# Optimization experiments

Measured on AMD Instinct MI355X. Metric: run time of the kernel, lower is better.

The kernel has to match this reference:

```python
import jax, jax.numpy as jnp
import numpy as np

N_NODES = 200000
N_EDGES = 800000
N_GRAPHS = 4096
IN_FEAT = 64
CONV_SIZES = [128, 128, 256, 256]
MAX_DEGREE = 5  # buckets 0..5 (degree clamped)
N_CLASSES = 2


def setup_inputs() -> dict:
    key = jax.random.key(0)
    ks = jax.random.split(key, 32)
    inp = {}
    inp["x"] = jax.random.normal(ks[0], (N_NODES, IN_FEAT), dtype=jnp.float32)
    inp["edge_index"] = jax.random.randint(ks[1], (2, N_EDGES), 0, N_NODES, dtype=jnp.int32)
    inp["batch"] = jnp.sort(jax.random.randint(ks[2], (N_NODES,), 0, N_GRAPHS, dtype=jnp.int32))
    # per-layer MFConv params: Wl (neighbor-sum branch, with bias), Wr (root branch, no bias),
    # one linear per degree bucket -> leading dim MAX_DEGREE+1
    c_in = IN_FEAT
    k = 3
    for li, c_out in enumerate(CONV_SIZES):
        s = 1.0 / np.sqrt(c_in)
        inp[f"Wl{li}"] = jax.random.normal(ks[k], (MAX_DEGREE + 1, c_in, c_out), dtype=jnp.float32) * s; k += 1
        inp[f"bl{li}"] = jax.random.normal(ks[k], (MAX_DEGREE + 1, c_out), dtype=jnp.float32) * 0.01; k += 1
        inp[f"Wr{li}"] = jax.random.normal(ks[k], (MAX_DEGREE + 1, c_in, c_out), dtype=jnp.float32) * s; k += 1
        c_in = c_out
    in_final = sum(CONV_SIZES) + CONV_SIZES[-1]  # concat of all layer outputs + pooled last layer
    inp["Wf"] = jax.random.normal(ks[k], (in_final, N_CLASSES), dtype=jnp.float32) * (1.0 / np.sqrt(in_final)); k += 1
    inp["bf"] = jax.random.normal(ks[k], (N_CLASSES,), dtype=jnp.float32) * 0.01
    return inp


def _mfconv(x, src, dst, deg, Wl, bl, Wr):
    # neighbor sum aggregation (source_to_target flow): msg_i = sum_{j->i} x_j
    msg = jax.ops.segment_sum(x[src], dst, num_segments=x.shape[0])  # [N, c_in]
    out = jnp.zeros((x.shape[0], Wl.shape[2]), dtype=x.dtype)
    for d in range(Wl.shape[0]):  # small fixed loop over degree buckets
        r = msg @ Wl[d] + bl[d] + x @ Wr[d]
        out = jnp.where((deg == d)[:, None], r, out)
    return out


def reference(x, edge_index, batch,
              Wl0, bl0, Wr0, Wl1, bl1, Wr1, Wl2, bl2, Wr2, Wl3, bl3, Wr3,
              Wf, bf):
    src, dst = edge_index[0], edge_index[1]
    n = x.shape[0]
    deg = jnp.clip(jnp.zeros((n,), jnp.int32).at[dst].add(1), 0, MAX_DEGREE)
    hs = []
    h = x
    for Wl, bl, Wr in ((Wl0, bl0, Wr0), (Wl1, bl1, Wr1), (Wl2, bl2, Wr2), (Wl3, bl3, Wr3)):
        h = _mfconv(h, src, dst, deg, Wl, bl, Wr)
        hs.append(h)
    # global_add_pool then repeat_interleave back to nodes == gather pooled by batch id
    h_pool = jax.ops.segment_sum(h, batch, num_segments=N_GRAPHS)  # [G, c_last]
    h_pool_ = h_pool[batch]  # [N, c_last]
    h_cat = jnp.concatenate(hs + [h_pool_], axis=1)  # [N, sum(sizes)+c_last]
    logits = h_cat @ Wf + bf
    return jax.nn.softmax(logits, axis=1)
```

## Files before the change

### kernel.cpp

```cpp
#include <hip/hip_runtime.h>
#include <cstdint>
#include <cstddef>

namespace {

constexpr int NN   = 200000;
constexpr int NE   = 800000;
constexpr int NG   = 4096;
constexpr int MAXD = 5;

constexpr int BM = 64;
constexpr int NBC = (NN + 255) / 256;
constexpr int NBLK  = (NN + BM - 1) / BM + 6;
constexpr int PERMN = NBLK * BM;

typedef _Float16 half8 __attribute__((ext_vector_type(8)));
typedef _Float16 half4 __attribute__((ext_vector_type(4)));
typedef _Float16 half2 __attribute__((ext_vector_type(2)));
typedef float    f32x4 __attribute__((ext_vector_type(4)));

constexpr size_t P_L0 = (size_t)6 * 128 * 128;
constexpr size_t P_L1 = (size_t)6 * 256 * 128;
constexpr size_t P_L2 = (size_t)6 * 256 * 256;
constexpr size_t P_L3 = (size_t)6 * 512 * 256;
constexpr size_t O_P0 = 0;
constexpr size_t O_P1 = O_P0 + P_L0;
constexpr size_t O_P2 = O_P1 + P_L1;
constexpr size_t O_P3 = O_P2 + P_L2;
constexpr size_t WTOT = O_P3 + P_L3;


__global__ void k_memset32(int* __restrict__ p, int v, int n) {
    int i = blockIdx.x * 256 + threadIdx.x;
    if (i < n) p[i] = v;
}

__global__ void k_report(float* __restrict__ outp, float v, int n) {
    int i = blockIdx.x * 256 + threadIdx.x;
    if (i < n) outp[i] = v;
}

template <int CIN, int COUT>
__global__ void k_wpack(const float* __restrict__ Wl, const float* __restrict__ Wr,
                        _Float16* __restrict__ hi, _Float16* __restrict__ lo) {
    constexpr int NT = CIN / 16;
    constexpr int NB = COUT / 16;
    const int total = 6 * NT * NB * 64;
    int idx = blockIdx.x * 256 + threadIdx.x;
    if (idx >= total) return;
    const int lane = idx & 63;
    int rest = idx >> 6;
    const int nb = rest % NB; rest /= NB;
    const int ti = rest % NT;
    const int d  = rest / NT;
    const int k0 = ti * 32 + ((lane >> 4) * 8);
    const int n  = nb * 16 + (lane & 15);
    half8 hv, lv;
#pragma unroll
    for (int j = 0; j < 8; j++) {
        const int kk = k0 + j;
        const float v = (kk < CIN)
                            ? Wl[((size_t)d * CIN + kk) * COUT + n]
                            : Wr[((size_t)d * CIN + (kk - CIN)) * COUT + n];
        const _Float16 h = (_Float16)v;
        hv[j] = h;
        lv[j] = (_Float16)(v - (float)h);
    }
    *(half8*)(hi + (size_t)idx * 8) = hv;
    *(half8*)(lo + (size_t)idx * 8) = lv;
}


__global__ void k_count_deg(const int* __restrict__ dst, int* __restrict__ deg) {
    int e = blockIdx.x * 256 + threadIdx.x;
    if (e < NE) atomicAdd(&deg[dst[e]], 1);
}

__global__ void k_scan_part(const int* __restrict__ deg, int* __restrict__ part) {
    __shared__ int s[256];
    int t = threadIdx.x, i = blockIdx.x * 256 + t;
    s[t] = (i < NN) ? deg[i] : 0;
    __syncthreads();
    for (int st = 128; st > 0; st >>= 1) {
        if (t < st) s[t] += s[t + st];
        __syncthreads();
    }
    if (t == 0) part[blockIdx.x] = s[0];
}

__global__ void k_scan_single(int* __restrict__ part, int nb) {
    __shared__ int s[1024];
    int t = threadIdx.x;
    int v0 = (t < nb) ? part[t] : 0;
    s[t] = v0;
    __syncthreads();
    for (int off = 1; off < 1024; off <<= 1) {
        int v = (t >= off) ? s[t - off] : 0;
        __syncthreads();
        s[t] += v;
        __syncthreads();
    }
    if (t < nb) part[t] = s[t] - v0;
}

__global__ void k_scan_final(const int* __restrict__ deg, const int* __restrict__ part,
                             int* __restrict__ row_ptr, int* __restrict__ cursor) {
    __shared__ int s[256];
    int t = threadIdx.x, i = blockIdx.x * 256 + t;
    int v0 = (i < NN) ? deg[i] : 0;
    s[t] = v0;
    __syncthreads();
    for (int off = 1; off < 256; off <<= 1) {
        int v = (t >= off) ? s[t - off] : 0;
        __syncthreads();
        s[t] += v;
        __syncthreads();
    }
    if (i < NN) {
        int excl = s[t] - v0 + part[blockIdx.x];
        row_ptr[i] = excl;
        cursor[i]  = excl;
        if (i == NN - 1) row_ptr[NN] = excl + v0;
    }
}

__global__ void k_fill_csr(const int* __restrict__ src, const int* __restrict__ dst,
                           int* __restrict__ cursor, int* __restrict__ col) {
    int e = blockIdx.x * 256 + threadIdx.x;
    if (e < NE) {
        int d = dst[e];
        int slot = atomicAdd(&cursor[d], 1);
        col[slot] = src[e];
    }
}


__global__ void k_bucket_blockcount(const int* __restrict__ deg, int* __restrict__ blkcnt) {
    __shared__ int h[6];
    int t = threadIdx.x;
    if (t < 6) h[t] = 0;
    __syncthreads();
    int i = blockIdx.x * 256 + t;
    if (i < NN) atomicAdd(&h[min(deg[i], MAXD)], 1);
    __syncthreads();
    if (t < 6) blkcnt[t * NBC + blockIdx.x] = h[t];
}

__global__ void k_bucket_scanall(int* __restrict__ blkcnt, int* __restrict__ bpad) {
    __shared__ int tot[6];
    int t = threadIdx.x;
    if (t < 6) {
        int run = 0;
        for (int j = 0; j < NBC; j++) {
            int v = blkcnt[t * NBC + j];
            blkcnt[t * NBC + j] = run;
            run += v;
        }
        tot[t] = run;
    }
    __syncthreads();
    if (t == 0) {
        int off = 0;
        for (int b = 0; b < 6; b++) {
            bpad[b] = off;
            off += ((tot[b] + BM - 1) / BM) * BM;
        }
        bpad[6] = off;
    }
}

__global__ void k_scatter2(const int* __restrict__ deg, const int* __restrict__ blkcnt,
                           const int* __restrict__ bpad, int* __restrict__ perm) {
    __shared__ int base[6];
    int t = threadIdx.x;
    if (t < 6) base[t] = bpad[t] + blkcnt[t * NBC + blockIdx.x];
    __syncthreads();
    int i = blockIdx.x * 256 + t;
    if (i < NN) {
        int b = min(deg[i], MAXD);
        int pos = atomicAdd(&base[b], 1);
        perm[pos] = i;
    }
}


__global__ void k_aggregate128(const float* __restrict__ hin, const int* __restrict__ row_ptr,
                               const int* __restrict__ col, float* __restrict__ msg) {
    int node = blockIdx.x * 4 + (threadIdx.x >> 6);
    int lane = threadIdx.x & 63;
    int s = row_ptr[node], e = row_ptr[node + 1];
    float2 acc = make_float2(0.f, 0.f);
    int p = s;
    for (; p + 4 <= e; p += 4) {
        const int c0 = col[p], c1 = col[p + 1], c2 = col[p + 2], c3 = col[p + 3];
        const float2 v0 = *(const float2*)(hin + (size_t)c0 * 128 + lane * 2);
        const float2 v1 = *(const float2*)(hin + (size_t)c1 * 128 + lane * 2);
        const float2 v2 = *(const float2*)(hin + (size_t)c2 * 128 + lane * 2);
        const float2 v3 = *(const float2*)(hin + (size_t)c3 * 128 + lane * 2);
        acc.x += (v0.x + v1.x) + (v2.x + v3.x);
        acc.y += (v0.y + v1.y) + (v2.y + v3.y);
    }
    for (; p < e; p++) {
        const float2 v = *(const float2*)(hin + (size_t)col[p] * 128 + lane * 2);
        acc.x += v.x; acc.y += v.y;
    }
    *(float2*)(msg + (size_t)node * 128 + lane * 2) = acc;
}

template <int C0, int C1, int COUT, int MINW, bool POOL_FUSE>
__launch_bounds__(512, MINW)
__global__ void k_transform(const float* __restrict__ hin0, const float* __restrict__ hin1,
                            const int* __restrict__ row_ptr, const int* __restrict__ col,
                            const _Float16* __restrict__ wph, const _Float16* __restrict__ wpl,
                            const float* __restrict__ bias, const float* __restrict__ Wf,
                            const int* __restrict__ perm, const int* __restrict__ deg,
                            const int* __restrict__ batch,
                            float* __restrict__ out0, float* __restrict__ pool,
                            float* __restrict__ logits, int wf_off) {
    constexpr int CIN = C0 + C1;
    constexpr int NW  = CIN / 32;
    constexpr int NT  = 2 * NW;
    constexpr int NB  = COUT / 16;
    constexpr int NTN = NB / 8;
    constexpr int CPL = CIN / 64;
    constexpr int PB_R = POOL_FUSE ? 64 : 1;

    struct FragBuf {
        _Float16 Ah[NW][4][64][8];
        _Float16 Al[NW][4][64][8];
    };
    union SMemU {
        FragBuf f;
        float pbuf[PB_R][COUT];
    };
    __shared__ SMemU sm;
    __shared__ int rowid[BM];
    __shared__ int gb[BM];
    __shared__ float lsx[BM], lsy[BM];

    const int t  = threadIdx.x;
    const int m0 = blockIdx.x * BM;

    if (t < BM) {
        rowid[t] = perm[m0 + t];
        lsx[t] = 0.f; lsy[t] = 0.f;
    }
    __syncthreads();
    if (rowid[0] < 0) return;

    const int d = min(deg[rowid[0]], MAXD);

    const int am = t & 63, wv = t >> 6;

    if constexpr (POOL_FUSE) {
        if (t < BM) gb[t] = (rowid[t] >= 0) ? batch[rowid[t]] : -1;
    }

    {
        const int kk = CPL * am;
        const bool lo_half = (C1 == 0) || (kk < C0);
        const float* gsrc = lo_half ? hin0 : hin1;
        const int    gst  = lo_half ? C0 : C1;
        const int    goff = lo_half ? kk : (kk - C0);
        const int ti = kk >> 5;
        const int o  = (kk >> 3) & 3;
        const int j0 = kk & 7;

#pragma unroll
        for (int i = 0; i < 8; i++) {
            const int r = wv * 8 + i;
            const int node = rowid[r];
            float a0 = 0.f, a1 = 0.f, a2 = 0.f, a3 = 0.f;
            if (node >= 0) {
                const int es = row_ptr[node], ee = row_ptr[node + 1];
                int p = es;
                for (; p + 4 <= ee; p += 4) {
                    const int c0 = col[p], c1 = col[p + 1];
                    const int c2 = col[p + 2], c3 = col[p + 3];
                    const float* r0 = gsrc + (size_t)c0 * gst + goff;
                    const float* r1 = gsrc + (size_t)c1 * gst + goff;
                    const float* r2 = gsrc + (size_t)c2 * gst + goff;
                    const float* r3 = gsrc + (size_t)c3 * gst + goff;
                    if constexpr (CPL == 4) {
                        f32x4 v0 = *(const f32x4*)r0, v1 = *(const f32x4*)r1;
                        f32x4 v2 = *(const f32x4*)r2, v3 = *(const f32x4*)r3;
                        v0 += v1; v2 += v3; v0 += v2;
                        a0 += v0[0]; a1 += v0[1]; a2 += v0[2]; a3 += v0[3];
                    } else if constexpr (CPL == 2) {
                        float2 v0 = *(const float2*)r0, v1 = *(const float2*)r1;
                        float2 v2 = *(const float2*)r2, v3 = *(const float2*)r3;
                        a0 += (v0.x + v1.x) + (v2.x + v3.x);
                        a1 += (v0.y + v1.y) + (v2.y + v3.y);
                    } else {
                        a0 += (*r0 + *r1) + (*r2 + *r3);
                    }
                }
                for (; p < ee; p++) {
                    const float* rr = gsrc + (size_t)col[p] * gst + goff;
                    if constexpr (CPL == 4) {
                        f32x4 v = *(const f32x4*)rr;
                        a0 += v[0]; a1 += v[1]; a2 += v[2]; a3 += v[3];
                    } else if constexpr (CPL == 2) {
                        float2 v = *(const float2*)rr;
                        a0 += v.x; a1 += v.y;
                    } else {
                        a0 += *rr;
                    }
                }
            }
            const int mt = r >> 4, rl = r & 15;
            if constexpr (CPL == 4) {
                half4 hv, lv;
                hv[0] = (_Float16)a0; lv[0] = (_Float16)(a0 - (float)hv[0]);
                hv[1] = (_Float16)a1; lv[1] = (_Float16)(a1 - (float)hv[1]);
                hv[2] = (_Float16)a2; lv[2] = (_Float16)(a2 - (float)hv[2]);
                hv[3] = (_Float16)a3; lv[3] = (_Float16)(a3 - (float)hv[3]);
                *(half4*)&sm.f.Ah[ti][mt][rl + 16 * o][j0] = hv;
                *(half4*)&sm.f.Al[ti][mt][rl + 16 * o][j0] = lv;
            } else if constexpr (CPL == 2) {
                half2 hv, lv;
                hv[0] = (_Float16)a0; lv[0] = (_Float16)(a0 - (float)hv[0]);
                hv[1] = (_Float16)a1; lv[1] = (_Float16)(a1 - (float)hv[1]);
                *(half2*)&sm.f.Ah[ti][mt][rl + 16 * o][j0] = hv;
                *(half2*)&sm.f.Al[ti][mt][rl + 16 * o][j0] = lv;
            } else {
                const _Float16 h = (_Float16)a0;
                sm.f.Ah[ti][mt][rl + 16 * o][j0] = h;
                sm.f.Al[ti][mt][rl + 16 * o][j0] = (_Float16)(a0 - (float)h);
            }
        }
    }
    __syncthreads();

    const int lx = t & 15, qd = (t >> 4) & 3;
    const int nb0 = wv * NTN;
    int rnode[4];
#pragma unroll
    for (int mt = 0; mt < 4; mt++) rnode[mt] = rowid[(am & 15) + 16 * mt];

    f32x4 acc[4][NTN];
#pragma unroll
    for (int mt = 0; mt < 4; mt++)
#pragma unroll
        for (int nt = 0; nt < NTN; nt++) acc[mt][nt] = (f32x4)0.f;

    for (int ti = 0; ti < NW; ti++) {
        half8 bh[NTN], bl[NTN];
        const size_t tbase = (((size_t)d * NT + ti) * NB) * 512;
#pragma unroll
        for (int nt = 0; nt < NTN; nt++) {
            const size_t off = tbase + (size_t)(nb0 + nt) * 512 + (size_t)am * 8;
            bh[nt] = *(const half8*)(wph + off);
            bl[nt] = *(const half8*)(wpl + off);
        }
        half8 ah[4], alo[4];
#pragma unroll
        for (int mt = 0; mt < 4; mt++) {
            ah[mt]  = *(const half8*)&sm.f.Ah[ti][mt][am][0];
            alo[mt] = *(const half8*)&sm.f.Al[ti][mt][am][0];
        }
#pragma unroll
        for (int nt = 0; nt < NTN; nt++)
#pragma unroll
            for (int mt = 0; mt < 4; mt++) {
                acc[mt][nt] = __builtin_amdgcn_mfma_f32_16x16x32_f16(ah[mt],  bh[nt], acc[mt][nt], 0, 0, 0);
                acc[mt][nt] = __builtin_amdgcn_mfma_f32_16x16x32_f16(alo[mt], bh[nt], acc[mt][nt], 0, 0, 0);
                acc[mt][nt] = __builtin_amdgcn_mfma_f32_16x16x32_f16(ah[mt],  bl[nt], acc[mt][nt], 0, 0, 0);
            }
    }
    for (int ti = NW; ti < NT; ti++) {
        half8 bh[NTN], bl[NTN];
        const size_t tbase = (((size_t)d * NT + ti) * NB) * 512;
#pragma unroll
        for (int nt = 0; nt < NTN; nt++) {
            const size_t off = tbase + (size_t)(nb0 + nt) * 512 + (size_t)am * 8;
            bh[nt] = *(const half8*)(wph + off);
            bl[nt] = *(const half8*)(wpl + off);
        }
        const int e = (ti - NW) * 32 + 8 * (am >> 4);
        f32x4 ra[4], rb[4];
#pragma unroll
        for (int mt = 0; mt < 4; mt++) {
            ra[mt] = (f32x4)0.f; rb[mt] = (f32x4)0.f;
            if (rnode[mt] >= 0) {
                const float* r = (C1 == 0 || e < C0)
                                     ? hin0 + (size_t)rnode[mt] * C0 + e
                                     : hin1 + (size_t)rnode[mt] * C1 + (e - C0);
                ra[mt] = *(const f32x4*)r;
                rb[mt] = *(const f32x4*)(r + 4);
            }
        }
        half8 ah[4], alo[4];
#pragma unroll
        for (int mt = 0; mt < 4; mt++) {
#pragma unroll
            for (int i = 0; i < 4; i++) {
                const _Float16 h0 = (_Float16)ra[mt][i];
                ah[mt][i] = h0;
                alo[mt][i] = (_Float16)(ra[mt][i] - (float)h0);
                const _Float16 h1 = (_Float16)rb[mt][i];
                ah[mt][4 + i] = h1;
                alo[mt][4 + i] = (_Float16)(rb[mt][i] - (float)h1);
            }
        }
#pragma unroll
        for (int nt = 0; nt < NTN; nt++)
#pragma unroll
            for (int mt = 0; mt < 4; mt++) {
                acc[mt][nt] = __builtin_amdgcn_mfma_f32_16x16x32_f16(ah[mt],  bh[nt], acc[mt][nt], 0, 0, 0);
                acc[mt][nt] = __builtin_amdgcn_mfma_f32_16x16x32_f16(alo[mt], bh[nt], acc[mt][nt], 0, 0, 0);
                acc[mt][nt] = __builtin_amdgcn_mfma_f32_16x16x32_f16(ah[mt],  bl[nt], acc[mt][nt], 0, 0, 0);
            }
    }

    float blv[NTN], w0[NTN], w1[NTN];
    int cols[NTN];
#pragma unroll
    for (int nt = 0; nt < NTN; nt++) {
        cols[nt] = wv * (16 * NTN) + nt * 16 + lx;
        blv[nt] = bias[d * COUT + cols[nt]];
        w0[nt]  = Wf[(size_t)(wf_off + cols[nt]) * 2 + 0];
        w1[nt]  = Wf[(size_t)(wf_off + cols[nt]) * 2 + 1];
    }

    __syncthreads();

#pragma unroll
    for (int mt = 0; mt < 4; mt++)
#pragma unroll
    for (int r = 0; r < 4; r++) {
        const int ri = mt * 16 + qd * 4 + r;
        const int node = rowid[ri];
        float p0 = 0.f, p1 = 0.f;
        float h[NTN];
#pragma unroll
        for (int nt = 0; nt < NTN; nt++) h[nt] = 0.f;
        if (node >= 0) {
#pragma unroll
            for (int nt = 0; nt < NTN; nt++) {
                h[nt] = acc[mt][nt][r] + blv[nt];
                p0 = fmaf(h[nt], w0[nt], p0);
                p1 = fmaf(h[nt], w1[nt], p1);
            }
            if constexpr (!POOL_FUSE) {
                float* orow = out0 + (size_t)node * COUT;
#pragma unroll
                for (int nt = 0; nt < NTN; nt++) orow[cols[nt]] = h[nt];
            }
        }
        if constexpr (POOL_FUSE) {
#pragma unroll
            for (int nt = 0; nt < NTN; nt++) sm.pbuf[ri][cols[nt]] = h[nt];
        }
#pragma unroll
        for (int s = 1; s < 16; s <<= 1) {
            p0 += __shfl_xor(p0, s, 64);
            p1 += __shfl_xor(p1, s, 64);
        }
        if (node >= 0 && lx == 0) {
            atomicAdd(&lsx[ri], p0);
            atomicAdd(&lsy[ri], p1);
        }
    }
    __syncthreads();

    if (t < BM) {
        const int node = rowid[t];
        if (node >= 0) {
            logits[(size_t)node * 2 + 0] += lsx[t];
            logits[(size_t)node * 2 + 1] += lsy[t];
        }
    }

    if constexpr (POOL_FUSE) {
        const int c  = t & 255;
        const int rh = t >> 8;
        float run = 0.f;
        int rg = -1;
        const int r0 = rh * 32, r1 = r0 + 32;
        for (int r = r0; r < r1; r++) {
            const int g = gb[r];
            if (g != rg) {
                if (rg >= 0) atomicAdd(&pool[(size_t)rg * 256 + c], run);
                run = 0.f; rg = g;
            }
            if (g >= 0) run += sm.pbuf[r][c];
        }
        if (rg >= 0) atomicAdd(&pool[(size_t)rg * 256 + c], run);
    }
}


__launch_bounds__(512, 4)
__global__ void k_gemm2b(float* __restrict__ buf0, float* __restrict__ buf1,
                         const _Float16* __restrict__ wph, const _Float16* __restrict__ wpl,
                         const float* __restrict__ bias, const float* __restrict__ Wf,
                         const int* __restrict__ perm, const int* __restrict__ deg,
                         float* __restrict__ logits) {
    constexpr int COUT = 256, NT = 8, NB = 16, NTN = 2;
    __shared__ _Float16 Ah[NT][4][64][8];
    __shared__ _Float16 Al[NT][4][64][8];
    __shared__ int rowid[BM];
    __shared__ float lsx[BM], lsy[BM];

    const int t  = threadIdx.x;
    const int m0 = blockIdx.x * BM;

    if (t < BM) {
        rowid[t] = perm[m0 + t];
        lsx[t] = 0.f; lsy[t] = 0.f;
    }
    __syncthreads();
    if (rowid[0] < 0) return;

    const int d = min(deg[rowid[0]], MAXD);

    const int am = t & 63, wv = t >> 6;

    {
        const int kk = 4 * am;
        const float* gsrc = (am < 32) ? buf0 : buf1;
        const int    goff = (am < 32) ? kk : (kk - 128);
        const int ti = am >> 3;
        const int o  = (am >> 1) & 3;
        const int j0 = 4 * (am & 1);
#pragma unroll
        for (int i = 0; i < 8; i++) {
            const int r = wv * 8 + i;
            const int node = rowid[r];
            f32x4 v = (f32x4)0.f;
            if (node >= 0) v = *(const f32x4*)(gsrc + (size_t)node * 128 + goff);
            const int mt = r >> 4, rl = r & 15;
            half4 hv, lv;
#pragma unroll
            for (int c = 0; c < 4; c++) {
                const _Float16 h = (_Float16)v[c];
                hv[c] = h; lv[c] = (_Float16)(v[c] - (float)h);
            }
            *(half4*)&Ah[ti][mt][rl + 16 * o][j0] = hv;
            *(half4*)&Al[ti][mt][rl + 16 * o][j0] = lv;
        }
    }
    __syncthreads();

    const int lx = t & 15, qd = (t >> 4) & 3;
    const int nb0 = wv * NTN;

    f32x4 acc[4][NTN];
#pragma unroll
    for (int mt = 0; mt < 4; mt++)
#pragma unroll
        for (int nt = 0; nt < NTN; nt++) acc[mt][nt] = (f32x4)0.f;

    for (int ti = 0; ti < NT; ti++) {
        half8 bh[NTN], bl[NTN];
        const size_t tbase = (((size_t)d * NT + ti) * NB) * 512;
#pragma unroll
        for (int nt = 0; nt < NTN; nt++) {
            const size_t off = tbase + (size_t)(nb0 + nt) * 512 + (size_t)am * 8;
            bh[nt] = *(const half8*)(wph + off);
            bl[nt] = *(const half8*)(wpl + off);
        }
        half8 ah[4], alo[4];
#pragma unroll
        for (int mt = 0; mt < 4; mt++) {
            ah[mt]  = *(const half8*)&Ah[ti][mt][am][0];
            alo[mt] = *(const half8*)&Al[ti][mt][am][0];
        }
#pragma unroll
        for (int nt = 0; nt < NTN; nt++)
#pragma unroll
            for (int mt = 0; mt < 4; mt++) {
                acc[mt][nt] = __builtin_amdgcn_mfma_f32_16x16x32_f16(ah[mt],  bh[nt], acc[mt][nt], 0, 0, 0);
                acc[mt][nt] = __builtin_amdgcn_mfma_f32_16x16x32_f16(alo[mt], bh[nt], acc[mt][nt], 0, 0, 0);
                acc[mt][nt] = __builtin_amdgcn_mfma_f32_16x16x32_f16(ah[mt],  bl[nt], acc[mt][nt], 0, 0, 0);
            }
    }

    float blv[NTN], w0[NTN], w1[NTN];
    int cols[NTN];
#pragma unroll
    for (int nt = 0; nt < NTN; nt++) {
        cols[nt] = wv * 32 + nt * 16 + lx;
        blv[nt] = bias[d * COUT + cols[nt]];
        w0[nt]  = Wf[(size_t)(256 + cols[nt]) * 2 + 0];
        w1[nt]  = Wf[(size_t)(256 + cols[nt]) * 2 + 1];
    }
#pragma unroll
    for (int mt = 0; mt < 4; mt++)
#pragma unroll
    for (int r = 0; r < 4; r++) {
        const int ri = mt * 16 + qd * 4 + r;
        const int node = rowid[ri];
        float p0 = 0.f, p1 = 0.f;
        if (node >= 0) {
#pragma unroll
            for (int nt = 0; nt < NTN; nt++) {
                const float h = acc[mt][nt][r] + blv[nt];
                p0 = fmaf(h, w0[nt], p0);
                p1 = fmaf(h, w1[nt], p1);
                if (cols[nt] < 128) buf0[(size_t)node * 128 + cols[nt]] = h;
                else                buf1[(size_t)node * 128 + cols[nt] - 128] = h;
            }
        }
#pragma unroll
        for (int s = 1; s < 16; s <<= 1) {
            p0 += __shfl_xor(p0, s, 64);
            p1 += __shfl_xor(p1, s, 64);
        }
        if (node >= 0 && lx == 0) {
            atomicAdd(&lsx[ri], p0);
            atomicAdd(&lsy[ri], p1);
        }
    }
    __syncthreads();
    if (t < BM) {
        const int node = rowid[t];
        if (node >= 0) {
            logits[(size_t)node * 2 + 0] += lsx[t];
            logits[(size_t)node * 2 + 1] += lsy[t];
        }
    }
}


__global__ void k_pool_logits(const float* __restrict__ pool, const float* __restrict__ Wf,
                              const float* __restrict__ bf, float* __restrict__ pl) {
    int g = blockIdx.x * 4 + (threadIdx.x >> 6);
    int lane = threadIdx.x & 63;
    const float* pr = pool + (size_t)g * 256;
    float p0 = 0.f, p1 = 0.f;
#pragma unroll
    for (int j = 0; j < 4; j++) {
        int k = lane + 64 * j;
        float v = pr[k];
        p0 = fmaf(v, Wf[(size_t)(768 + k) * 2 + 0], p0);
        p1 = fmaf(v, Wf[(size_t)(768 + k) * 2 + 1], p1);
    }
#pragma unroll
    for (int s = 1; s < 64; s <<= 1) {
        p0 += __shfl_xor(p0, s, 64);
        p1 += __shfl_xor(p1, s, 64);
    }
    if (lane == 0) {
        pl[(size_t)g * 2 + 0] = p0 + bf[0];
        pl[(size_t)g * 2 + 1] = p1 + bf[1];
    }
}

__global__ void k_final(const float* __restrict__ logits, const float* __restrict__ pl,
                        const int* __restrict__ batch, float* __restrict__ outp) {
    int i = blockIdx.x * 256 + threadIdx.x;
    if (i < NN) {
        int g = batch[i];
        float l0 = logits[(size_t)i * 2 + 0] + pl[(size_t)g * 2 + 0];
        float l1 = logits[(size_t)i * 2 + 1] + pl[(size_t)g * 2 + 1];
        float m = fmaxf(l0, l1);
        float e0 = expf(l0 - m), e1 = expf(l1 - m);
        float inv = 1.f / (e0 + e1);
        outp[(size_t)i * 2 + 0] = e0 * inv;
        outp[(size_t)i * 2 + 1] = e1 * inv;
    }
}

}

extern "C" void kernel_launch(void* const* d_in, const int* in_sizes, int n_in,
                              void* d_out, int out_size, void* d_ws, size_t ws_size,
                              hipStream_t stream) {
    const float* x     = (const float*)d_in[0];
    const int*   ei    = (const int*)d_in[1];
    const int*   batch = (const int*)d_in[2];
    const float* Wl0 = (const float*)d_in[3];  const float* bl0 = (const float*)d_in[4];
    const float* Wr0 = (const float*)d_in[5];
    const float* Wl1 = (const float*)d_in[6];  const float* bl1 = (const float*)d_in[7];
    const float* Wr1 = (const float*)d_in[8];
    const float* Wl2 = (const float*)d_in[9];  const float* bl2 = (const float*)d_in[10];
    const float* Wr2 = (const float*)d_in[11];
    const float* Wl3 = (const float*)d_in[12]; const float* bl3 = (const float*)d_in[13];
    const float* Wr3 = (const float*)d_in[14];
    const float* Wf  = (const float*)d_in[15]; const float* bf  = (const float*)d_in[16];
    const int* src = ei;
    const int* dst = ei + NE;
    float* outp = (float*)d_out;
    (void)in_sizes; (void)n_in;

    char* w = (char*)d_ws;
    auto alloc = [&](size_t bytes) -> void* {
        void* p = (void*)w;
        w += (bytes + 255) & ~(size_t)255;
        return p;
    };
    int*   deg    = (int*)alloc((size_t)NN * 4);
    float* logits = (float*)alloc((size_t)NN * 2 * 4);
    float* pool   = (float*)alloc((size_t)NG * 256 * 4);
    size_t zero_words = (size_t)(w - (char*)deg) / 4;
    int*   bpad    = (int*)alloc(32);
    int*   blkcnt  = (int*)alloc((size_t)6 * NBC * 4);
    int*   perm    = (int*)alloc((size_t)PERMN * 4);
    int*   row_ptr = (int*)alloc((size_t)(NN + 1) * 4);
    int*   cursor  = (int*)alloc((size_t)NN * 4);
    int*   col     = (int*)alloc((size_t)NE * 4);
    int*   part    = (int*)alloc(1024 * 4);
    float* pl      = (float*)alloc((size_t)NG * 2 * 4);
    _Float16* whi  = (_Float16*)alloc(WTOT * 2);
    _Float16* wlo  = (_Float16*)alloc(WTOT * 2);
    float* bufA    = (float*)alloc((size_t)NN * 128 * 4);
    float* bufB    = (float*)alloc((size_t)NN * 128 * 4);

    size_t required = (size_t)(w - (char*)d_ws);
    if (required > ws_size) {
        k_report<<<(out_size + 255) / 256, 256, 0, stream>>>(
            outp, (float)(double)(ws_size >> 20), out_size);
        return;
    }

    dim3 b256(256);
    dim3 b512(512);
    k_memset32<<<(int)((zero_words + 255) / 256), b256, 0, stream>>>((int*)deg, 0, (int)zero_words);
    k_memset32<<<(PERMN + 255) / 256, b256, 0, stream>>>(perm, -1, PERMN);

    k_wpack<64, 128><<<(int)(P_L0 / 8 + 255) / 256, b256, 0, stream>>>(Wl0, Wr0, whi + O_P0, wlo + O_P0);
    k_wpack<128, 128><<<(int)(P_L1 / 8 + 255) / 256, b256, 0, stream>>>(Wl1, Wr1, whi + O_P1, wlo + O_P1);
    k_wpack<128, 256><<<(int)(P_L2 / 8 + 255) / 256, b256, 0, stream>>>(Wl2, Wr2, whi + O_P2, wlo + O_P2);
    k_wpack<256, 256><<<(int)(P_L3 / 8 + 255) / 256, b256, 0, stream>>>(Wl3, Wr3, whi + O_P3, wlo + O_P3);

    k_count_deg<<<NE / 256, b256, 0, stream>>>(dst, deg);
    k_scan_part<<<NBC, b256, 0, stream>>>(deg, part);
    k_scan_single<<<1, 1024, 0, stream>>>(part, NBC);
    k_scan_final<<<NBC, b256, 0, stream>>>(deg, part, row_ptr, cursor);
    k_fill_csr<<<NE / 256, b256, 0, stream>>>(src, dst, cursor, col);
    k_bucket_blockcount<<<NBC, b256, 0, stream>>>(deg, blkcnt);
    k_bucket_scanall<<<1, 64, 0, stream>>>(blkcnt, bpad);
    k_scatter2<<<NBC, b256, 0, stream>>>(deg, blkcnt, bpad, perm);

    k_transform<64, 0, 128, 4, false><<<dim3(NBLK), b512, 0, stream>>>(
        x, nullptr, row_ptr, col, whi + O_P0, wlo + O_P0,
        bl0, Wf, perm, deg, nullptr, bufA, nullptr, logits, 0);
    k_transform<128, 0, 128, 4, false><<<dim3(NBLK), b512, 0, stream>>>(
        bufA, nullptr, row_ptr, col, whi + O_P1, wlo + O_P1,
        bl1, Wf, perm, deg, nullptr, bufB, nullptr, logits, 128);
    k_aggregate128<<<NN / 4, b256, 0, stream>>>(bufB, row_ptr, col, bufA);
    k_gemm2b<<<dim3(NBLK), b512, 0, stream>>>(
        bufA, bufB, whi + O_P2, wlo + O_P2, bl2, Wf, perm, deg, logits);
    k_transform<128, 128, 256, 4, true><<<dim3(NBLK), b512, 0, stream>>>(
        bufA, bufB, row_ptr, col, whi + O_P3, wlo + O_P3,
        bl3, Wf, perm, deg, batch, nullptr, pool, logits, 512);

    k_pool_logits<<<NG / 4, b256, 0, stream>>>(pool, Wf, bf, pl);
    k_final<<<NBC, b256, 0, stream>>>(logits, pl, batch, outp);
}
```

Measured before the change: 1.370 ms.

## Stage root features via LDS fragments, drop LDS atomics, pad pool buffer

The root-branch operand is now loaded cooperatively with coalesced per-row vector loads, split into hi/lo halves and written into the shared fragment buffer. The second MFMA loop then reads A fragments from LDS instead of doing strided per-lane global gathers and in-register conversion. Logit partials are written to per-wave shared slots and summed once per row, replacing shared atomics, and the pool staging buffer is padded to reduce bank conflicts. This adds two extra block barriers and more shared memory.

```diff
diff --git a/kernel.cpp b/kernel.cpp
--- a/kernel.cpp
+++ b/kernel.cpp
@@ -224,6 +224,7 @@
     constexpr int NTN = NB / 8;
     constexpr int CPL = CIN / 64;
     constexpr int PB_R = POOL_FUSE ? 64 : 1;
+    constexpr int PB_C = 258;
 
     struct FragBuf {
         _Float16 Ah[NW][4][64][8];
@@ -231,20 +232,17 @@
     };
     union SMemU {
         FragBuf f;
-        float pbuf[PB_R][COUT];
+        float pbuf[PB_R][PB_C];
     };
     __shared__ SMemU sm;
     __shared__ int rowid[BM];
     __shared__ int gb[BM];
-    __shared__ float lsx[BM], lsy[BM];
+    __shared__ float lsx[8][BM], lsy[8][BM];
 
     const int t  = threadIdx.x;
     const int m0 = blockIdx.x * BM;
 
-    if (t < BM) {
-        rowid[t] = perm[m0 + t];
-        lsx[t] = 0.f; lsy[t] = 0.f;
-    }
+    if (t < BM) rowid[t] = perm[m0 + t];
     __syncthreads();
     if (rowid[0] < 0) return;
 
@@ -256,16 +254,16 @@
         if (t < BM) gb[t] = (rowid[t] >= 0) ? batch[rowid[t]] : -1;
     }
 
+    const int kk = CPL * am;
+    const bool lo_half = (C1 == 0) || (kk < C0);
+    const float* gsrc = lo_half ? hin0 : hin1;
+    const int    gst  = lo_half ? C0 : C1;
+    const int    goff = lo_half ? kk : (kk - C0);
+    const int ti0 = kk >> 5;
+    const int o0  = (kk >> 3) & 3;
+    const int j00 = kk & 7;
+
     {
-        const int kk = CPL * am;
-        const bool lo_half = (C1 == 0) || (kk < C0);
-        const float* gsrc = lo_half ? hin0 : hin1;
-        const int    gst  = lo_half ? C0 : C1;
-        const int    goff = lo_half ? kk : (kk - C0);
-        const int ti = kk >> 5;
-        const int o  = (kk >> 3) & 3;
-        const int j0 = kk & 7;
-
 #pragma unroll
         for (int i = 0; i < 8; i++) {
             const int r = wv * 8 + i;
@@ -315,18 +313,18 @@
                 hv[1] = (_Float16)a1; lv[1] = (_Float16)(a1 - (float)hv[1]);
                 hv[2] = (_Float16)a2; lv[2] = (_Float16)(a2 - (float)hv[2]);
                 hv[3] = (_Float16)a3; lv[3] = (_Float16)(a3 - (float)hv[3]);
-                *(half4*)&sm.f.Ah[ti][mt][rl + 16 * o][j0] = hv;
-                *(half4*)&sm.f.Al[ti][mt][rl + 16 * o][j0] = lv;
+                *(half4*)&sm.f.Ah[ti0][mt][rl + 16 * o0][j00] = hv;
+                *(half4*)&sm.f.Al[ti0][mt][rl + 16 * o0][j00] = lv;
             } else if constexpr (CPL == 2) {
                 half2 hv, lv;
                 hv[0] = (_Float16)a0; lv[0] = (_Float16)(a0 - (float)hv[0]);
                 hv[1] = (_Float16)a1; lv[1] = (_Float16)(a1 - (float)hv[1]);
-                *(half2*)&sm.f.Ah[ti][mt][rl + 16 * o][j0] = hv;
-                *(half2*)&sm.f.Al[ti][mt][rl + 16 * o][j0] = lv;
+                *(half2*)&sm.f.Ah[ti0][mt][rl + 16 * o0][j00] = hv;
+                *(half2*)&sm.f.Al[ti0][mt][rl + 16 * o0][j00] = lv;
             } else {
                 const _Float16 h = (_Float16)a0;
-                sm.f.Ah[ti][mt][rl + 16 * o][j0] = h;
-                sm.f.Al[ti][mt][rl + 16 * o][j0] = (_Float16)(a0 - (float)h);
+                sm.f.Ah[ti0][mt][rl + 16 * o0][j00] = h;
+                sm.f.Al[ti0][mt][rl + 16 * o0][j00] = (_Float16)(a0 - (float)h);
             }
         }
     }
@@ -334,9 +332,6 @@
 
     const int lx = t & 15, qd = (t >> 4) & 3;
     const int nb0 = wv * NTN;
-    int rnode[4];
-#pragma unroll
-    for (int mt = 0; mt < 4; mt++) rnode[mt] = rowid[(am & 15) + 16 * mt];
 
     f32x4 acc[4][NTN];
 #pragma unroll
@@ -368,40 +363,58 @@
                 acc[mt][nt] = __builtin_amdgcn_mfma_f32_16x16x32_f16(ah[mt],  bl[nt], acc[mt][nt], 0, 0, 0);
             }
     }
-    for (int ti = NW; ti < NT; ti++) {
+    __syncthreads();
+
+    {
+#pragma unroll
+        for (int i = 0; i < 8; i++) {
+            const int r = wv * 8 + i;
+            const int node = rowid[r];
+            const int mt = r >> 4, rl = r & 15;
+            if constexpr (CPL == 4) {
+                f32x4 v = (f32x4)0.f;
+                if (node >= 0) v = *(const f32x4*)(gsrc + (size_t)node * gst + goff);
+                half4 hv, lv;
+#pragma unroll
+                for (int c = 0; c < 4; c++) {
+                    const _Float16 h = (_Float16)v[c];
+                    hv[c] = h; lv[c] = (_Float16)(v[c] - (float)h);
+                }
+                *(half4*)&sm.f.Ah[ti0][mt][rl + 16 * o0][j00] = hv;
+                *(half4*)&sm.f.Al[ti0][mt][rl + 16 * o0][j00] = lv;
+            } else if constexpr (CPL == 2) {
+                float2 v = make_float2(0.f, 0.f);
+                if (node >= 0) v = *(const float2*)(gsrc + (size_t)node * gst + goff);
+                half2 hv, lv;
+                hv[0] = (_Float16)v.x; lv[0] = (_Float16)(v.x - (float)hv[0]);
+                hv[1] = (_Float16)v.y; lv[1] = (_Float16)(v.y - (float)hv[1]);
+                *(half2*)&sm.f.Ah[ti0][mt][rl + 16 * o0][j00] = hv;
+                *(half2*)&sm.f.Al[ti0][mt][rl + 16 * o0][j00] = lv;
+            } else {
+                float v = 0.f;
+                if (node >= 0) v = gsrc[(size_t)node * gst + goff];
+                const _Float16 h = (_Float16)v;
+                sm.f.Ah[ti0][mt][rl + 16 * o0][j00] = h;
+                sm.f.Al[ti0][mt][rl + 16 * o0][j00] = (_Float16)(v - (float)h);
+            }
+        }
+    }
+    __syncthreads();
+
+    for (int ti = 0; ti < NW; ti++) {
         half8 bh[NTN], bl[NTN];
-        const size_t tbase = (((size_t)d * NT + ti) * NB) * 512;
+        const size_t tbase = (((size_t)d * NT + NW + ti) * NB) * 512;
 #pragma unroll
         for (int nt = 0; nt < NTN; nt++) {
             const size_t off = tbase + (size_t)(nb0 + nt) * 512 + (size_t)am * 8;
             bh[nt] = *(const half8*)(wph + off);
             bl[nt] = *(const half8*)(wpl + off);
         }
-        const int e = (ti - NW) * 32 + 8 * (am >> 4);
-        f32x4 ra[4], rb[4];
+        half8 ah[4], alo[4];
 #pragma unroll
         for (int mt = 0; mt < 4; mt++) {
-            ra[mt] = (f32x4)0.f; rb[mt] = (f32x4)0.f;
-            if (rnode[mt] >= 0) {
-                const float* r = (C1 == 0 || e < C0)
-                                     ? hin0 + (size_t)rnode[mt] * C0 + e
-                                     : hin1 + (size_t)rnode[mt] * C1 + (e - C0);
-                ra[mt] = *(const f32x4*)r;
-                rb[mt] = *(const f32x4*)(r + 4);
-            }
-        }
-        half8 ah[4], alo[4];
-#pragma unroll
-        for (int mt = 0; mt < 4; mt++) {
-#pragma unroll
-            for (int i = 0; i < 4; i++) {
-                const _Float16 h0 = (_Float16)ra[mt][i];
-                ah[mt][i] = h0;
-                alo[mt][i] = (_Float16)(ra[mt][i] - (float)h0);
-                const _Float16 h1 = (_Float16)rb[mt][i];
-                ah[mt][4 + i] = h1;
-                alo[mt][4 + i] = (_Float16)(rb[mt][i] - (float)h1);
-            }
+            ah[mt]  = *(const half8*)&sm.f.Ah[ti][mt][am][0];
+            alo[mt] = *(const half8*)&sm.f.Al[ti][mt][am][0];
         }
 #pragma unroll
         for (int nt = 0; nt < NTN; nt++)
@@ -457,9 +470,9 @@
             p0 += __shfl_xor(p0, s, 64);
             p1 += __shfl_xor(p1, s, 64);
         }
-        if (node >= 0 && lx == 0) {
-            atomicAdd(&lsx[ri], p0);
-            atomicAdd(&lsy[ri], p1);
+        if (lx == 0) {
+            lsx[wv][ri] = p0;
+            lsy[wv][ri] = p1;
         }
     }
     __syncthreads();
@@ -467,8 +480,11 @@
     if (t < BM) {
         const int node = rowid[t];
         if (node >= 0) {
-            logits[(size_t)node * 2 + 0] += lsx[t];
-            logits[(size_t)node * 2 + 1] += lsy[t];
+            float sx = 0.f, sy = 0.f;
+#pragma unroll
+            for (int w = 0; w < 8; w++) { sx += lsx[w][t]; sy += lsy[w][t]; }
+            logits[(size_t)node * 2 + 0] += sx;
+            logits[(size_t)node * 2 + 1] += sy;
         }
     }
 
@@ -501,15 +517,12 @@
     __shared__ _Float16 Ah[NT][4][64][8];
     __shared__ _Float16 Al[NT][4][64][8];
     __shared__ int rowid[BM];
-    __shared__ float lsx[BM], lsy[BM];
+    __shared__ float lsx[8][BM], lsy[8][BM];
 
     const int t  = threadIdx.x;
     const int m0 = blockIdx.x * BM;
 
-    if (t < BM) {
-        rowid[t] = perm[m0 + t];
-        lsx[t] = 0.f; lsy[t] = 0.f;
-    }
+    if (t < BM) rowid[t] = perm[m0 + t];
     __syncthreads();
     if (rowid[0] < 0) return;
 
@@ -608,17 +621,20 @@
             p0 += __shfl_xor(p0, s, 64);
             p1 += __shfl_xor(p1, s, 64);
         }
-        if (node >= 0 && lx == 0) {
-            atomicAdd(&lsx[ri], p0);
-            atomicAdd(&lsy[ri], p1);
+        if (lx == 0) {
+            lsx[wv][ri] = p0;
+            lsy[wv][ri] = p1;
         }
     }
     __syncthreads();
     if (t < BM) {
         const int node = rowid[t];
         if (node >= 0) {
-            logits[(size_t)node * 2 + 0] += lsx[t];
-            logits[(size_t)node * 2 + 1] += lsy[t];
+            float sx = 0.f, sy = 0.f;
+#pragma unroll
+            for (int w = 0; w < 8; w++) { sx += lsx[w][t]; sy += lsy[w][t]; }
+            logits[(size_t)node * 2 + 0] += sx;
+            logits[(size_t)node * 2 + 1] += sy;
         }
     }
 }
```

Measured after the change: 1.209 ms, median of 2. 1.13x faster.
